# Kernel optimization log

Hardware: AMD Instinct MI355X
Metric: run time of the kernel (lower is better)

The kernel has to match this reference:

```python
import jax, jax.numpy as jnp
import numpy as np
import math

N_FREQ = 50
ENC_DIM = 4 * N_FREQ  # 200
D = 5
N_GENES = 1000
N_CELLS = 5000
N_FRAG = 200_000


def sine_encoding(coords):
    # frequencies: [f1,f1,f2,f2,...] length 2*N_FREQ; shifts: [0, pi/2, 0, pi/2, ...]
    i = jnp.arange(1, N_FREQ + 1, dtype=jnp.float32)
    freqs = jnp.repeat(1.0 / jnp.power(jnp.float32(1000.0), 2.0 * i / N_FREQ), 2)
    shifts = jnp.tile(jnp.array([0.0, math.pi / 2], jnp.float32), N_FREQ)
    # coords [F,2] -> [F,2,2*nf] -> [F,4*nf]
    return jnp.sin((coords[..., None] * freqs + shifts).reshape(coords.shape[0], -1))


def self_attention(x):
    # x: [G, i, D]; NOTE: scale uses sqrt(seq_len) = sqrt(x.shape[-2]) as in the original
    scores = jnp.einsum('gid,gjd->gij', x, x) / jnp.sqrt(jnp.float32(x.shape[1]))
    w = jax.nn.softmax(scores, axis=-1)
    return jnp.einsum('gij,gjd->gid', w, x)


def setup_inputs() -> dict:
    key = jax.random.key(0)
    ks = jax.random.split(key, 6)
    coordinates = jax.random.uniform(ks[0], (N_FRAG, 2), jnp.float32, -1000.0, 1000.0)
    genemapping = jax.random.randint(ks[1], (N_FRAG,), 0, N_GENES)
    local_cellxgene_ix = jax.random.randint(ks[2], (N_FRAG,), 0, N_CELLS * N_GENES)
    genes_oi = jnp.arange(N_GENES)
    # ragged groups: disjoint fragment index sets for group sizes 2, 3, 4
    n2 = jnp.arange(60000)             # 30000 pairs
    n3 = jnp.arange(60000) + 60000     # 20000 triples
    n4 = jnp.arange(60000) + 120000    # 15000 quads
    stdv = 1.0 / math.sqrt(D)
    weight1_frag = jax.random.uniform(ks[3], (N_GENES, ENC_DIM, D), jnp.float32, -stdv, stdv)
    weight1_expr = jnp.ones((N_GENES, D), jnp.float32)
    bias1 = jax.random.normal(ks[4], (N_GENES,), jnp.float32)  # mean_gene_expression
    return dict(coordinates=coordinates, genemapping=genemapping, n2=n2, n3=n3, n4=n4,
                local_cellxgene_ix=local_cellxgene_ix, genes_oi=genes_oi,
                weight1_frag=weight1_frag, weight1_expr=weight1_expr, bias1=bias1)


def reference(coordinates, genemapping, n2, n3, n4, local_cellxgene_ix, genes_oi,
              weight1_frag, weight1_expr, bias1):
    # FragmentEmbedder: sine encode, per-gene weight gather, contract, sigmoid
    enc = sine_encoding(coordinates)                                 # [F, 200]
    emb = jax.nn.sigmoid(jnp.einsum('fe,fed->fd', enc, weight1_frag[genemapping]))  # [F, 5]
    # ragged self-attention over fixed-size groups (2, 3, 4)
    for idx, i in ((n2, 2), (n3, 3), (n4, 4)):
        x = emb[idx].reshape(-1, i, D)
        emb = emb.at[idx].set(self_attention(x).reshape(-1, D))
    # EmbeddingGenePooler: segment sum over cell x gene
    pooled = jax.ops.segment_sum(emb, local_cellxgene_ix, num_segments=N_CELLS * N_GENES)
    cell_gene_embedding = pooled.reshape(N_CELLS, N_GENES, D)
    # EmbeddingToExpression: gene-wise weighted sum + mean expression bias
    return (cell_gene_embedding * weight1_expr[genes_oi]).sum(-1) + bias1[genes_oi]
```

## Files before the change

kernel.cpp:

```cpp
#include <hip/hip_runtime.h>
#include <math.h>

#define DD 5
#define EST 8
#define NFREQ 50
#define NB 128

__global__ __launch_bounds__(256) void hist_init_kernel(
    const int* __restrict__ gm, int F, int chunk,
    int* __restrict__ bc, int n_genes, int* __restrict__ done,
    float* __restrict__ out, const float* __restrict__ bias,
    const int* __restrict__ genes_oi, int n_cells) {
  __shared__ int cnt[1000];
  __shared__ float s_brow[1000];
  const int tid = threadIdx.x;
  if (blockIdx.x == 0 && tid == 0) *done = 0;
  for (int j = tid; j < n_genes; j += blockDim.x) {
    s_brow[j] = bias[genes_oi[j]];
    cnt[j] = 0;
  }
  __syncthreads();
  if (blockIdx.x < NB) {
    int lo = blockIdx.x * chunk;
    int hi = min(F, lo + chunk);
    for (int i = lo + tid; i < hi; i += blockDim.x)
      atomicAdd(&cnt[gm[i]], 1);
  }
  const float4* b4 = (const float4*)s_brow;
  const int q = n_genes >> 2;
  for (int c = blockIdx.x; c < n_cells; c += gridDim.x) {
    float4* dst = (float4*)out + (size_t)c * q;
    for (int t = tid; t < q; t += blockDim.x) dst[t] = b4[t];
  }
  __syncthreads();
  if (blockIdx.x < NB)
    for (int j = tid; j < n_genes; j += blockDim.x)
      bc[j * NB + blockIdx.x] = cnt[j];
}

__global__ __launch_bounds__(256) void binscan_starts_kernel(
    int* __restrict__ bc, int n_genes, int* __restrict__ totals,
    int* __restrict__ starts, int* __restrict__ done, int nblocks) {
  __shared__ int s_amlast;
  __shared__ int s_ws[4];
  int lane = threadIdx.x & 63;
  int wv = threadIdx.x >> 6;
  int bin = blockIdx.x * 4 + wv;
  if (bin < n_genes) {
    int2* row = (int2*)(bc + (size_t)bin * NB);
    int2 v = row[lane];
    int p = v.x + v.y;
    int ip = p;
#pragma unroll
    for (int off = 1; off < 64; off <<= 1) {
      int q = __shfl_up(ip, off);
      if (lane >= off) ip += q;
    }
    int base = ip - p;
    int2 e;
    e.x = base;
    e.y = base + v.x;
    row[lane] = e;
    if (lane == 63) totals[bin] = ip;
  }
  __syncthreads();
  if (threadIdx.x == 0) {
    __threadfence();
    int tk = atomicAdd(done, 1);
    s_amlast = (tk == nblocks - 1);
  }
  __syncthreads();
  if (!s_amlast) return;
  __threadfence();
  int t = threadIdx.x;
  int4 v = make_int4(0, 0, 0, 0);
  if (4 * t < n_genes) v = ((const int4*)totals)[t];
  int p = v.x + v.y + v.z + v.w;
  int ip = p;
#pragma unroll
  for (int off = 1; off < 64; off <<= 1) {
    int q = __shfl_up(ip, off);
    if (lane >= off) ip += q;
  }
  if (lane == 63) s_ws[wv] = ip;
  __syncthreads();
  int add = 0;
#pragma unroll
  for (int i = 0; i < 4; ++i)
    if (i < wv) add += s_ws[i];
  int excl = add + ip - p;
  int4 e;
  e.x = excl;
  e.y = excl + v.x;
  e.z = e.y + v.y;
  e.w = e.z + v.z;
  if (4 * t < n_genes) ((int4*)starts)[t] = e;
  if (4 * t + 4 == n_genes) starts[n_genes] = e.w + v.w;
}

__global__ __launch_bounds__(256) void blockscatter_kernel(
    const int* __restrict__ gm, int F, int chunk,
    const int* __restrict__ bc, const int* __restrict__ starts,
    int* __restrict__ order, int n_genes) {
  __shared__ int cur[1000];
  int b = blockIdx.x;
  for (int j = threadIdx.x; j < n_genes; j += blockDim.x)
    cur[j] = starts[j] + bc[j * NB + b];
  __syncthreads();
  int lo = b * chunk;
  int hi = min(F, lo + chunk);
  for (int i = lo + threadIdx.x; i < hi; i += blockDim.x) {
    int g = gm[i];
    int p = atomicAdd(&cur[g], 1);
    order[p] = i;
  }
}

__global__ __launch_bounds__(256) void embed_kernel(
    const float2* __restrict__ coords, const int* __restrict__ order,
    const int* __restrict__ starts, const float* __restrict__ W,
    float* __restrict__ emb, int n_genes,
    const int* __restrict__ lci, const int* __restrict__ genes_oi,
    const float* __restrict__ wexpr, float* __restrict__ out) {
  __shared__ float s_w[1000];
  __shared__ float s_freq[NFREQ];
  const int tid = threadIdx.x;
  if (tid < NFREQ)
    s_freq[tid] = exp2f(-0.39863137f * (float)(tid + 1));
  int g = blockIdx.x;
  const float* __restrict__ Wg = W + (size_t)g * (4 * NFREQ * DD);
  for (int idx = tid; idx < 1000; idx += blockDim.x) {
    int k = idx / 20, r = idx % 20;
    s_w[idx] = (r < 10) ? Wg[10 * k + r] : Wg[500 + 10 * k + (r - 10)];
  }
  __syncthreads();
  int s0 = starts[g];
  int s1 = starts[g + 1];
  const float4* __restrict__ w4 = (const float4*)s_w;

  for (int i = s0 + tid; i < s1; i += blockDim.x) {
    int f = order[i];
    float2 xy = coords[f];
    float a0 = 0.f, a1 = 0.f, a2 = 0.f, a3 = 0.f, a4 = 0.f;
#pragma unroll 2
    for (int k = 0; k < NFREQ; ++k) {
      float fr = s_freq[k];
      float ax = xy.x * fr;
      float ay = xy.y * fr;
      float sx = __sinf(ax), cx = __cosf(ax);
      float sy = __sinf(ay), cy = __cosf(ay);
      float4 c0 = w4[5 * k + 0];
      float4 c1 = w4[5 * k + 1];
      float4 c2 = w4[5 * k + 2];
      float4 c3 = w4[5 * k + 3];
      float4 c4 = w4[5 * k + 4];
      a0 += sx * c0.x + cx * c1.y + sy * c2.z + cy * c3.w;
      a1 += sx * c0.y + cx * c1.z + sy * c2.w + cy * c4.x;
      a2 += sx * c0.z + cx * c1.w + sy * c3.x + cy * c4.y;
      a3 += sx * c0.w + cx * c2.x + sy * c3.y + cy * c4.z;
      a4 += sx * c1.x + cx * c2.y + sy * c3.z + cy * c4.w;
    }
    float x0 = 1.f / (1.f + __expf(-a0));
    float x1 = 1.f / (1.f + __expf(-a1));
    float x2 = 1.f / (1.f + __expf(-a2));
    float x3 = 1.f / (1.f + __expf(-a3));
    float x4 = 1.f / (1.f + __expf(-a4));
    float* e = emb + (size_t)f * EST;
    float4 r;
    r.x = x0; r.y = x1; r.z = x2; r.w = x3;
    *reinterpret_cast<float4*>(e) = r;
    e[4] = x4;
    int ix = lci[f];
    const float* w = wexpr + (size_t)genes_oi[ix % n_genes] * DD;
    float s = x0 * w[0] + x1 * w[1] + x2 * w[2] + x3 * w[3] + x4 * w[4];
    atomicAdd(out + ix, s);
  }
}

template <int SZ>
__device__ __forceinline__ void attn_row_delta(const int* __restrict__ grp,
                                               int a,
                                               const float* __restrict__ emb,
                                               const int* __restrict__ lci,
                                               const int* __restrict__ genes_oi,
                                               const float* __restrict__ wexpr,
                                               int n_genes, float* __restrict__ out) {
  int fid[SZ];
  float x[SZ][DD];
#pragma unroll
  for (int b = 0; b < SZ; ++b) {
    fid[b] = grp[b];
    const float* p = emb + (size_t)fid[b] * EST;
    float4 v = *reinterpret_cast<const float4*>(p);
    x[b][0] = v.x; x[b][1] = v.y; x[b][2] = v.z; x[b][3] = v.w;
    x[b][4] = p[4];
  }
  const float scale = rsqrtf((float)SZ);
  float sc[SZ];
  float m = -1e30f;
#pragma unroll
  for (int b = 0; b < SZ; ++b) {
    float dt = 0.f;
#pragma unroll
    for (int d = 0; d < DD; ++d) dt += x[a][d] * x[b][d];
    sc[b] = dt * scale;
    m = fmaxf(m, sc[b]);
  }
  float sum = 0.f;
#pragma unroll
  for (int b = 0; b < SZ; ++b) {
    sc[b] = __expf(sc[b] - m);
    sum += sc[b];
  }
  float inv = 1.f / sum;
  int ix = lci[fid[a]];
  int g = genes_oi[ix % n_genes];
  const float* w = wexpr + (size_t)g * DD;
  float s = 0.f;
#pragma unroll
  for (int d = 0; d < DD; ++d) {
    float acc = 0.f;
#pragma unroll
    for (int b = 0; b < SZ; ++b) acc += sc[b] * x[b][d];
    s += (acc * inv - x[a][d]) * w[d];
  }
  atomicAdd(out + ix, s);
}

__global__ __launch_bounds__(256) void attn_delta_kernel(
    const int* __restrict__ n2, int c2,
    const int* __restrict__ n3, int c3,
    const int* __restrict__ n4, int c4,
    const float* __restrict__ emb, const int* __restrict__ lci,
    const int* __restrict__ genes_oi, const float* __restrict__ wexpr,
    int n_genes, float* __restrict__ out) {
  int gtid = blockIdx.x * blockDim.x + threadIdx.x;
  int gs = gridDim.x * blockDim.x;
  int rtot = c2 + c3 + c4;
  for (int r = gtid; r < rtot; r += gs) {
    if (r < c2) {
      int rb = r & ~1;
      attn_row_delta<2>(n2 + rb, r & 1, emb, lci, genes_oi, wexpr, n_genes, out);
    } else if (r < c2 + c3) {
      unsigned rp = (unsigned)(r - c2);
      unsigned grp = rp / 3u;
      int a = (int)(rp - grp * 3u);
      attn_row_delta<3>(n3 + grp * 3u, a, emb, lci, genes_oi, wexpr, n_genes, out);
    } else {
      int rp = r - c2 - c3;
      int rb = rp & ~3;
      attn_row_delta<4>(n4 + rb, rp & 3, emb, lci, genes_oi, wexpr, n_genes, out);
    }
  }
}

extern "C" void kernel_launch(void* const* d_in, const int* in_sizes, int n_in,
                              void* d_out, int out_size, void* d_ws, size_t ws_size,
                              hipStream_t stream) {
  const float2* coords  = (const float2*)d_in[0];
  const int* gm         = (const int*)d_in[1];
  const int* n2         = (const int*)d_in[2];
  const int* n3         = (const int*)d_in[3];
  const int* n4         = (const int*)d_in[4];
  const int* lci        = (const int*)d_in[5];
  const int* genes_oi   = (const int*)d_in[6];
  const float* W        = (const float*)d_in[7];
  const float* wexpr    = (const float*)d_in[8];
  const float* bias     = (const float*)d_in[9];
  float* out            = (float*)d_out;

  const int F       = in_sizes[1];
  const int n_genes = in_sizes[6];
  const int c2 = in_sizes[2];
  const int c3 = in_sizes[3];
  const int c4 = in_sizes[4];

  char* ws = (char*)d_ws;
  size_t off = 0;
  float* emb   = (float*)(ws + off); off += (size_t)F * EST * sizeof(float);
  int* order   = (int*)(ws + off);   off += (size_t)F * sizeof(int);
  int* bc      = (int*)(ws + off);   off += (size_t)n_genes * NB * sizeof(int);
  off = (off + 15) & ~(size_t)15;
  int* starts  = (int*)(ws + off);   off += (size_t)(n_genes + 4) * sizeof(int);
  off = (off + 15) & ~(size_t)15;
  int* totals  = (int*)(ws + off);   off += (size_t)n_genes * sizeof(int);
  int* done    = (int*)(ws + off);   off += 4 * sizeof(int);

  const int tb = 256;
  const int chunk = (F + NB - 1) / NB;
  const int n_cells = out_size / n_genes;

  hist_init_kernel<<<1024, tb, 0, stream>>>(gm, F, chunk, bc, n_genes, done,
                                            out, bias, genes_oi, n_cells);
  int scan_blocks = (n_genes + 3) / 4;
  binscan_starts_kernel<<<scan_blocks, tb, 0, stream>>>(bc, n_genes, totals,
                                                        starts, done, scan_blocks);
  blockscatter_kernel<<<NB, tb, 0, stream>>>(gm, F, chunk, bc, starts, order, n_genes);
  embed_kernel<<<n_genes, tb, 0, stream>>>(coords, order, starts, W, emb, n_genes,
                                           lci, genes_oi, wexpr, out);
  int rtot = c2 + c3 + c4;
  int ablocks = (rtot + tb - 1) / tb;
  attn_delta_kernel<<<ablocks, tb, 0, stream>>>(n2, c2, n3, c3, n4, c4,
                                                emb, lci, genes_oi, wexpr,
                                                n_genes, out);
}
```

Measured before the change: 136.5 us.

## Map one wavefront per gene and process four fragments per lane in embed

The embed kernel now gives each 64-lane wavefront its own gene, with four genes per block, instead of one 256-thread block per gene. Each lane handles four fragments at once, so every shared-memory weight load in the frequency loop is reused across four fragments. The aim is to cut LDS traffic per fragment and reduce the lanes left idle when a gene has about 200 fragments. The cost is more registers per lane and shared memory grown to 16 KB, and genes with more than 256 fragments loop again with partly masked lanes.

```diff
diff --git a/kernel.cpp b/kernel.cpp
--- a/kernel.cpp
+++ b/kernel.cpp
@@ -122,58 +122,82 @@
     float* __restrict__ emb, int n_genes,
     const int* __restrict__ lci, const int* __restrict__ genes_oi,
     const float* __restrict__ wexpr, float* __restrict__ out) {
-  __shared__ float s_w[1000];
+  __shared__ float s_w[4][1000];
   __shared__ float s_freq[NFREQ];
   const int tid = threadIdx.x;
+  const int lane = tid & 63;
+  const int wv = tid >> 6;
   if (tid < NFREQ)
     s_freq[tid] = exp2f(-0.39863137f * (float)(tid + 1));
-  int g = blockIdx.x;
-  const float* __restrict__ Wg = W + (size_t)g * (4 * NFREQ * DD);
-  for (int idx = tid; idx < 1000; idx += blockDim.x) {
-    int k = idx / 20, r = idx % 20;
-    s_w[idx] = (r < 10) ? Wg[10 * k + r] : Wg[500 + 10 * k + (r - 10)];
-  }
-  __syncthreads();
-  int s0 = starts[g];
-  int s1 = starts[g + 1];
-  const float4* __restrict__ w4 = (const float4*)s_w;
-
-  for (int i = s0 + tid; i < s1; i += blockDim.x) {
-    int f = order[i];
-    float2 xy = coords[f];
-    float a0 = 0.f, a1 = 0.f, a2 = 0.f, a3 = 0.f, a4 = 0.f;
-#pragma unroll 2
+  const int g = blockIdx.x * 4 + wv;
+  if (g < n_genes) {
+    const float* __restrict__ Wg = W + (size_t)g * (4 * NFREQ * DD);
+    for (int idx = lane; idx < 1000; idx += 64) {
+      int k = idx / 20, r = idx % 20;
+      s_w[wv][idx] = (r < 10) ? Wg[10 * k + r] : Wg[500 + 10 * k + (r - 10)];
+    }
+  }
+  __syncthreads();
+  if (g >= n_genes) return;
+  const int s0 = starts[g];
+  const int s1 = starts[g + 1];
+  const float4* __restrict__ w4 = (const float4*)s_w[wv];
+
+  for (int base = s0; base < s1; base += 256) {
+    int fid[4];
+    float2 xy[4];
+    bool act[4];
+#pragma unroll
+    for (int b = 0; b < 4; ++b) {
+      int i = base + 64 * b + lane;
+      act[b] = (i < s1);
+      fid[b] = act[b] ? order[i] : 0;
+      xy[b] = act[b] ? coords[fid[b]] : make_float2(0.f, 0.f);
+    }
+    float acc[4][5];
+#pragma unroll
+    for (int b = 0; b < 4; ++b)
+#pragma unroll
+      for (int d = 0; d < 5; ++d) acc[b][d] = 0.f;
+
     for (int k = 0; k < NFREQ; ++k) {
       float fr = s_freq[k];
-      float ax = xy.x * fr;
-      float ay = xy.y * fr;
-      float sx = __sinf(ax), cx = __cosf(ax);
-      float sy = __sinf(ay), cy = __cosf(ay);
       float4 c0 = w4[5 * k + 0];
       float4 c1 = w4[5 * k + 1];
       float4 c2 = w4[5 * k + 2];
       float4 c3 = w4[5 * k + 3];
       float4 c4 = w4[5 * k + 4];
-      a0 += sx * c0.x + cx * c1.y + sy * c2.z + cy * c3.w;
-      a1 += sx * c0.y + cx * c1.z + sy * c2.w + cy * c4.x;
-      a2 += sx * c0.z + cx * c1.w + sy * c3.x + cy * c4.y;
-      a3 += sx * c0.w + cx * c2.x + sy * c3.y + cy * c4.z;
-      a4 += sx * c1.x + cx * c2.y + sy * c3.z + cy * c4.w;
-    }
-    float x0 = 1.f / (1.f + __expf(-a0));
-    float x1 = 1.f / (1.f + __expf(-a1));
-    float x2 = 1.f / (1.f + __expf(-a2));
-    float x3 = 1.f / (1.f + __expf(-a3));
-    float x4 = 1.f / (1.f + __expf(-a4));
-    float* e = emb + (size_t)f * EST;
-    float4 r;
-    r.x = x0; r.y = x1; r.z = x2; r.w = x3;
-    *reinterpret_cast<float4*>(e) = r;
-    e[4] = x4;
-    int ix = lci[f];
-    const float* w = wexpr + (size_t)genes_oi[ix % n_genes] * DD;
-    float s = x0 * w[0] + x1 * w[1] + x2 * w[2] + x3 * w[3] + x4 * w[4];
-    atomicAdd(out + ix, s);
+#pragma unroll
+      for (int b = 0; b < 4; ++b) {
+        float ax = xy[b].x * fr;
+        float ay = xy[b].y * fr;
+        float sx = __sinf(ax), cx = __cosf(ax);
+        float sy = __sinf(ay), cy = __cosf(ay);
+        acc[b][0] += sx * c0.x + cx * c1.y + sy * c2.z + cy * c3.w;
+        acc[b][1] += sx * c0.y + cx * c1.z + sy * c2.w + cy * c4.x;
+        acc[b][2] += sx * c0.z + cx * c1.w + sy * c3.x + cy * c4.y;
+        acc[b][3] += sx * c0.w + cx * c2.x + sy * c3.y + cy * c4.z;
+        acc[b][4] += sx * c1.x + cx * c2.y + sy * c3.z + cy * c4.w;
+      }
+    }
+#pragma unroll
+    for (int b = 0; b < 4; ++b) {
+      if (!act[b]) continue;
+      float x0 = 1.f / (1.f + __expf(-acc[b][0]));
+      float x1 = 1.f / (1.f + __expf(-acc[b][1]));
+      float x2 = 1.f / (1.f + __expf(-acc[b][2]));
+      float x3 = 1.f / (1.f + __expf(-acc[b][3]));
+      float x4 = 1.f / (1.f + __expf(-acc[b][4]));
+      float* e = emb + (size_t)fid[b] * EST;
+      float4 r;
+      r.x = x0; r.y = x1; r.z = x2; r.w = x3;
+      *reinterpret_cast<float4*>(e) = r;
+      e[4] = x4;
+      int ix = lci[fid[b]];
+      const float* w = wexpr + (size_t)genes_oi[ix % n_genes] * DD;
+      float s = x0 * w[0] + x1 * w[1] + x2 * w[2] + x3 * w[3] + x4 * w[4];
+      atomicAdd(out + ix, s);
+    }
   }
 }
 
@@ -296,8 +320,9 @@
   binscan_starts_kernel<<<scan_blocks, tb, 0, stream>>>(bc, n_genes, totals,
                                                         starts, done, scan_blocks);
   blockscatter_kernel<<<NB, tb, 0, stream>>>(gm, F, chunk, bc, starts, order, n_genes);
-  embed_kernel<<<n_genes, tb, 0, stream>>>(coords, order, starts, W, emb, n_genes,
-                                           lci, genes_oi, wexpr, out);
+  int embed_blocks = (n_genes + 3) / 4;
+  embed_kernel<<<embed_blocks, tb, 0, stream>>>(coords, order, starts, W, emb,
+                                                n_genes, lci, genes_oi, wexpr, out);
   int rtot = c2 + c3 + c4;
   int ablocks = (rtot + tb - 1) / tb;
   attn_delta_kernel<<<ablocks, tb, 0, stream>>>(n2, c2, n3, c3, n4, c4,
```

Result: slower. 145.5 us (+6.5%).
